# Performance work log

Measured on AMD Instinct MI355X. Metric: run time of the kernel, lower is better.

## Reference

```python
import jax, jax.numpy as jnp
import numpy as np

K1, K2 = 0.01, 0.03
DATA_RANGE = 1.0
EPS = 1e-6


def setup_inputs() -> dict:
    key = jax.random.key(0)
    k1, k2, k3 = jax.random.split(key, 3)
    B, C, H, W = 4, 3, 256, 176
    S, M = 5, 18
    X = jax.random.normal(k1, (B, C, H, W), dtype=jnp.float32)
    Y = jax.random.normal(k2, (B, C, H, W), dtype=jnp.float32)
    bp_mask = jax.random.uniform(k3, (B, S, M, H, W), dtype=jnp.float32)
    return {"X": X, "Y": Y, "bp_mask": bp_mask}


def reference(X, Y, bp_mask):
    # Rescale from [-1, 1] to [0, 1]
    X = (X + 1.0) / 2.0
    Y = (Y + 1.0) / 2.0
    C1 = (K1 * DATA_RANGE) ** 2
    C2 = (K2 * DATA_RANGE) ** 2

    # Normalized mask weights: [B, S, M, H, W]
    msum = bp_mask.sum(axis=(-2, -1), keepdims=True)
    w = bp_mask / (msum + EPS)

    # Masked first / second moments -> [B, S, M, C], no repeated 6D tensors
    mu1 = jnp.einsum('bchw,bsmhw->bsmc', X, w)
    mu2 = jnp.einsum('bchw,bsmhw->bsmc', Y, w)
    mu11 = jnp.einsum('bchw,bsmhw->bsmc', X * X, w)
    mu22 = jnp.einsum('bchw,bsmhw->bsmc', Y * Y, w)
    mu12 = jnp.einsum('bchw,bsmhw->bsmc', X * Y, w)

    mu1_sq = mu1 * mu1
    mu2_sq = mu2 * mu2
    mu1_mu2 = mu1 * mu2
    sigma1_sq = mu11 - mu1_sq
    sigma2_sq = mu22 - mu2_sq
    sigma12 = mu12 - mu1_mu2

    cs = (2.0 * sigma12 + C2) / (sigma1_sq + sigma2_sq + C2)
    ssim = (2.0 * mu1_mu2 + C1) / (mu1_sq + mu2_sq + C1) * cs
    # nonnegative_ssim=True
    ssim = jax.nn.relu(ssim)
    cs = jax.nn.relu(cs)

    # Mean over merged (M, C) axis -> [B, S]
    cs_batch = cs.mean(axis=(2, 3))
    ssim_batch = ssim.mean(axis=(2, 3))

    msssim = jnp.prod(cs_batch[:, :-1], axis=1) * ssim_batch[:, -1]
    return msssim.mean()
```

## Files before the change

### kernel.cpp

```cpp
#include <hip/hip_runtime.h>

#define B_  4
#define C_  3
#define S_  5
#define M_  18
#define HW  45056
#define HW4 (HW/4)
#define SPLIT 4
#define TPB 256
#define CHUNK4 (HW4/SPLIT)
#define ITERS (CHUNK4/TPB)
#define NPLANE (B_*S_*M_)

#define ACC1(WC, XC, YC, c) do { \
    float xs = fmaf((XC), 0.5f, 0.5f); \
    float ys = fmaf((YC), 0.5f, 0.5f); \
    float wx = (WC) * xs; \
    float wy = (WC) * ys; \
    a1[c]  = fmaf((WC), xs, a1[c]); \
    a2[c]  = fmaf((WC), ys, a2[c]); \
    a11[c] = fmaf(wx, xs, a11[c]); \
    a22[c] = fmaf(wy, ys, a22[c]); \
    a12[c] = fmaf(wx, ys, a12[c]); \
  } while (0)

__global__ __launch_bounds__(TPB) void moments_kernel(
    const float4* __restrict__ X, const float4* __restrict__ Y,
    const float4* __restrict__ Mk, float* __restrict__ part) {
  int bid   = blockIdx.x;
  int plane = bid / SPLIT;
  int chunk = bid - plane * SPLIT;
  int b     = plane / (S_ * M_);

  const float4* mp = Mk + (size_t)plane * HW4;
  const float4* xp = X  + (size_t)b * (C_ * HW4);
  const float4* yp = Y  + (size_t)b * (C_ * HW4);

  int base = chunk * CHUNK4 + (int)threadIdx.x;

  float aW = 0.f;
  float a1[C_], a2[C_], a11[C_], a22[C_], a12[C_];
#pragma unroll
  for (int c = 0; c < C_; ++c) { a1[c]=a2[c]=a11[c]=a22[c]=a12[c]=0.f; }

#pragma unroll
  for (int it = 0; it < ITERS; ++it) {
    int i = base + it * TPB;
    float4 w = mp[i];
    aW += (w.x + w.y) + (w.z + w.w);
#pragma unroll
    for (int c = 0; c < C_; ++c) {
      float4 xv = xp[c * HW4 + i];
      float4 yv = yp[c * HW4 + i];
      ACC1(w.x, xv.x, yv.x, c);
      ACC1(w.y, xv.y, yv.y, c);
      ACC1(w.z, xv.z, yv.z, c);
      ACC1(w.w, xv.w, yv.w, c);
    }
  }

  float v[16];
  v[0] = aW;
#pragma unroll
  for (int c = 0; c < C_; ++c) {
    v[1 + c*5 + 0] = a1[c];
    v[1 + c*5 + 1] = a2[c];
    v[1 + c*5 + 2] = a11[c];
    v[1 + c*5 + 3] = a22[c];
    v[1 + c*5 + 4] = a12[c];
  }

#pragma unroll
  for (int off = 32; off > 0; off >>= 1) {
#pragma unroll
    for (int j = 0; j < 16; ++j) v[j] += __shfl_xor(v[j], off);
  }

  __shared__ float red[TPB/64][16];
  int lane = threadIdx.x & 63;
  int wv   = threadIdx.x >> 6;
  if (lane == 0) {
#pragma unroll
    for (int j = 0; j < 16; ++j) red[wv][j] = v[j];
  }
  __syncthreads();
  if (threadIdx.x < 16) {
    float s = (red[0][threadIdx.x] + red[1][threadIdx.x]) +
              (red[2][threadIdx.x] + red[3][threadIdx.x]);
    part[(size_t)bid * 16 + threadIdx.x] = s;
  }
}

__global__ __launch_bounds__(384) void finalize_kernel(
    const float* __restrict__ part, float* __restrict__ out) {
  __shared__ float csS[NPLANE], ssS[NPLANE];
  __shared__ double csb[B_*S_], ssb[B_*S_];
  int t = threadIdx.x;

  if (t < NPLANE) {
    double s[16];
#pragma unroll
    for (int j = 0; j < 16; ++j) s[j] = 0.0;
    for (int ch = 0; ch < SPLIT; ++ch) {
      const float* p = part + (size_t)(t * SPLIT + ch) * 16;
#pragma unroll
      for (int j = 0; j < 16; ++j) s[j] += (double)p[j];
    }
    const double C1d = 1e-4, C2d = 9e-4;
    double inv = 1.0 / (s[0] + 1e-6);
    double csAcc = 0.0, ssAcc = 0.0;
#pragma unroll
    for (int c = 0; c < C_; ++c) {
      double mu1  = s[1 + c*5 + 0] * inv;
      double mu2  = s[1 + c*5 + 1] * inv;
      double mu11 = s[1 + c*5 + 2] * inv;
      double mu22 = s[1 + c*5 + 3] * inv;
      double mu12 = s[1 + c*5 + 4] * inv;
      double m1s = mu1*mu1, m2s = mu2*mu2, m12 = mu1*mu2;
      double sig1  = mu11 - m1s;
      double sig2  = mu22 - m2s;
      double sig12 = mu12 - m12;
      double cs   = (2.0*sig12 + C2d) / (sig1 + sig2 + C2d);
      double ssim = (2.0*m12 + C1d) / (m1s + m2s + C1d) * cs;
      if (cs   < 0.0) cs   = 0.0;
      if (ssim < 0.0) ssim = 0.0;
      csAcc += cs; ssAcc += ssim;
    }
    csS[t] = (float)csAcc;
    ssS[t] = (float)ssAcc;
  }
  __syncthreads();

  if (t < B_*S_) {
    double cb = 0.0, sb = 0.0;
    for (int m = 0; m < M_; ++m) { cb += (double)csS[t*M_ + m]; sb += (double)ssS[t*M_ + m]; }
    csb[t] = cb / (double)(M_*C_);
    ssb[t] = sb / (double)(M_*C_);
  }
  __syncthreads();

  if (t == 0) {
    double acc = 0.0;
    for (int b = 0; b < B_; ++b) {
      double p = ssb[b*S_ + (S_-1)];
      for (int s = 0; s < S_-1; ++s) p *= csb[b*S_ + s];
      acc += p;
    }
    out[0] = (float)(acc / (double)B_);
  }
}

extern "C" void kernel_launch(void* const* d_in, const int* in_sizes, int n_in,
                              void* d_out, int out_size, void* d_ws, size_t ws_size,
                              hipStream_t stream) {
  (void)in_sizes; (void)n_in; (void)out_size; (void)ws_size;
  const float4* X  = (const float4*)d_in[0];
  const float4* Y  = (const float4*)d_in[1];
  const float4* Mk = (const float4*)d_in[2];
  float* part = (float*)d_ws;
  float* out  = (float*)d_out;

  hipLaunchKernelGGL(moments_kernel, dim3(NPLANE*SPLIT), dim3(TPB), 0, stream,
                     X, Y, Mk, part);
  hipLaunchKernelGGL(finalize_kernel, dim3(1), dim3(384), 0, stream, part, out);
}
```

Measured before the change: 117.8 us.

## Process three mask planes per block to reuse X/Y loads

Each block now handles a group of three mask planes, so X and Y loads and their rescaling are shared across three planes instead of being reloaded for each one. The split count rises from 4 to 11, which keeps the grid size similar, and the finalize kernel reindexes the partial sums to match. The cost is higher register pressure from 48 accumulators per thread, longer shuffle reductions, and fewer loop iterations per thread.

```diff
diff --git a/kernel.cpp b/kernel.cpp
--- a/kernel.cpp
+++ b/kernel.cpp
@@ -6,88 +6,94 @@
 #define M_  18
 #define HW  45056
 #define HW4 (HW/4)
-#define SPLIT 4
+#define G_  3
+#define GPBS (M_/G_)
+#define NGROUP (B_*S_*GPBS)
+#define SPLIT 11
 #define TPB 256
 #define CHUNK4 (HW4/SPLIT)
 #define ITERS (CHUNK4/TPB)
+#define NV (G_*16)
 #define NPLANE (B_*S_*M_)
-
-#define ACC1(WC, XC, YC, c) do { \
-    float xs = fmaf((XC), 0.5f, 0.5f); \
-    float ys = fmaf((YC), 0.5f, 0.5f); \
-    float wx = (WC) * xs; \
-    float wy = (WC) * ys; \
-    a1[c]  = fmaf((WC), xs, a1[c]); \
-    a2[c]  = fmaf((WC), ys, a2[c]); \
-    a11[c] = fmaf(wx, xs, a11[c]); \
-    a22[c] = fmaf(wy, ys, a22[c]); \
-    a12[c] = fmaf(wx, ys, a12[c]); \
-  } while (0)
 
 __global__ __launch_bounds__(TPB) void moments_kernel(
     const float4* __restrict__ X, const float4* __restrict__ Y,
     const float4* __restrict__ Mk, float* __restrict__ part) {
   int bid   = blockIdx.x;
-  int plane = bid / SPLIT;
-  int chunk = bid - plane * SPLIT;
-  int b     = plane / (S_ * M_);
+  int g     = bid / SPLIT;
+  int chunk = bid - g * SPLIT;
+  int bs    = g / GPBS;
+  int gm    = g - bs * GPBS;
+  int b     = bs / S_;
 
-  const float4* mp = Mk + (size_t)plane * HW4;
+  const float4* mp = Mk + (size_t)(bs * M_ + gm * G_) * HW4;
   const float4* xp = X  + (size_t)b * (C_ * HW4);
   const float4* yp = Y  + (size_t)b * (C_ * HW4);
 
   int base = chunk * CHUNK4 + (int)threadIdx.x;
 
-  float aW = 0.f;
-  float a1[C_], a2[C_], a11[C_], a22[C_], a12[C_];
+  float acc[NV];
 #pragma unroll
-  for (int c = 0; c < C_; ++c) { a1[c]=a2[c]=a11[c]=a22[c]=a12[c]=0.f; }
+  for (int j = 0; j < NV; ++j) acc[j] = 0.f;
 
 #pragma unroll
   for (int it = 0; it < ITERS; ++it) {
     int i = base + it * TPB;
-    float4 w = mp[i];
-    aW += (w.x + w.y) + (w.z + w.w);
+    float4 wv[G_], xv[C_], yv[C_];
+#pragma unroll
+    for (int j = 0; j < G_; ++j) wv[j] = mp[j * HW4 + i];
+#pragma unroll
+    for (int c = 0; c < C_; ++c) { xv[c] = xp[c * HW4 + i]; yv[c] = yp[c * HW4 + i]; }
+
+    float xs[C_][4], ys[C_][4];
 #pragma unroll
     for (int c = 0; c < C_; ++c) {
-      float4 xv = xp[c * HW4 + i];
-      float4 yv = yp[c * HW4 + i];
-      ACC1(w.x, xv.x, yv.x, c);
-      ACC1(w.y, xv.y, yv.y, c);
-      ACC1(w.z, xv.z, yv.z, c);
-      ACC1(w.w, xv.w, yv.w, c);
+      xs[c][0] = fmaf(xv[c].x, 0.5f, 0.5f); ys[c][0] = fmaf(yv[c].x, 0.5f, 0.5f);
+      xs[c][1] = fmaf(xv[c].y, 0.5f, 0.5f); ys[c][1] = fmaf(yv[c].y, 0.5f, 0.5f);
+      xs[c][2] = fmaf(xv[c].z, 0.5f, 0.5f); ys[c][2] = fmaf(yv[c].z, 0.5f, 0.5f);
+      xs[c][3] = fmaf(xv[c].w, 0.5f, 0.5f); ys[c][3] = fmaf(yv[c].w, 0.5f, 0.5f);
     }
-  }
 
-  float v[16];
-  v[0] = aW;
 #pragma unroll
-  for (int c = 0; c < C_; ++c) {
-    v[1 + c*5 + 0] = a1[c];
-    v[1 + c*5 + 1] = a2[c];
-    v[1 + c*5 + 2] = a11[c];
-    v[1 + c*5 + 3] = a22[c];
-    v[1 + c*5 + 4] = a12[c];
+    for (int j = 0; j < G_; ++j) {
+      float w4[4] = { wv[j].x, wv[j].y, wv[j].z, wv[j].w };
+      float* a = acc + j * 16;
+#pragma unroll
+      for (int k = 0; k < 4; ++k) {
+        float wk = w4[k];
+        a[0] += wk;
+#pragma unroll
+        for (int c = 0; c < C_; ++c) {
+          float xsv = xs[c][k], ysv = ys[c][k];
+          float wx = wk * xsv, wy = wk * ysv;
+          a[1 + c*5 + 0] = fmaf(wk, xsv, a[1 + c*5 + 0]);
+          a[1 + c*5 + 1] = fmaf(wk, ysv, a[1 + c*5 + 1]);
+          a[1 + c*5 + 2] = fmaf(wx, xsv, a[1 + c*5 + 2]);
+          a[1 + c*5 + 3] = fmaf(wy, ysv, a[1 + c*5 + 3]);
+          a[1 + c*5 + 4] = fmaf(wx, ysv, a[1 + c*5 + 4]);
+        }
+      }
+    }
   }
 
 #pragma unroll
   for (int off = 32; off > 0; off >>= 1) {
 #pragma unroll
-    for (int j = 0; j < 16; ++j) v[j] += __shfl_xor(v[j], off);
+    for (int j = 0; j < NV; ++j) acc[j] += __shfl_xor(acc[j], off);
   }
 
-  __shared__ float red[TPB/64][16];
+  __shared__ float red[TPB/64][NV];
   int lane = threadIdx.x & 63;
-  int wv   = threadIdx.x >> 6;
+  int wv_  = threadIdx.x >> 6;
   if (lane == 0) {
 #pragma unroll
-    for (int j = 0; j < 16; ++j) red[wv][j] = v[j];
+    for (int j = 0; j < NV; ++j) red[wv_][j] = acc[j];
   }
   __syncthreads();
-  if (threadIdx.x < 16) {
+  if (threadIdx.x < NV) {
     float s = (red[0][threadIdx.x] + red[1][threadIdx.x]) +
               (red[2][threadIdx.x] + red[3][threadIdx.x]);
-    part[(size_t)bid * 16 + threadIdx.x] = s;
+    part[(size_t)bid * NV + threadIdx.x] = s;
   }
 }
 
@@ -98,14 +104,21 @@
   int t = threadIdx.x;
 
   if (t < NPLANE) {
+    int bs = t / M_;
+    int m  = t - bs * M_;
+    int gm = m / G_;
+    int j  = m - gm * G_;
+    int g  = bs * GPBS + gm;
+
     double s[16];
 #pragma unroll
-    for (int j = 0; j < 16; ++j) s[j] = 0.0;
+    for (int v = 0; v < 16; ++v) s[v] = 0.0;
     for (int ch = 0; ch < SPLIT; ++ch) {
-      const float* p = part + (size_t)(t * SPLIT + ch) * 16;
+      const float* p = part + (size_t)(g * SPLIT + ch) * NV + j * 16;
 #pragma unroll
-      for (int j = 0; j < 16; ++j) s[j] += (double)p[j];
+      for (int v = 0; v < 16; ++v) s[v] += (double)p[v];
     }
+
     const double C1d = 1e-4, C2d = 9e-4;
     double inv = 1.0 / (s[0] + 1e-6);
     double csAcc = 0.0, ssAcc = 0.0;
@@ -160,7 +173,7 @@
   float* part = (float*)d_ws;
   float* out  = (float*)d_out;
 
-  hipLaunchKernelGGL(moments_kernel, dim3(NPLANE*SPLIT), dim3(TPB), 0, stream,
+  hipLaunchKernelGGL(moments_kernel, dim3(NGROUP*SPLIT), dim3(TPB), 0, stream,
                      X, Y, Mk, part);
   hipLaunchKernelGGL(finalize_kernel, dim3(1), dim3(384), 0, stream, part, out);
 }
```

Result: slower. 121.0 us (+2.7%).

## Group six mask planes per block to share X/Y loads, fuse finalize via last-block atomic

Applied to the files above, without the earlier changes.

Each block now holds six waves, and each wave handles a different mask plane over the same spatial chunk. The X/Y reads for that chunk are therefore shared across planes through cache rather than reloaded for every plane. Each wave writes its own partial directly, and a global atomic counter lets the last block run the finalize step, which removes the second kernel launch. The cost is an added memset, an atomic and threadfences per block, and a finalize that runs serially at the tail of the grid.

```diff
diff --git a/kernel.cpp b/kernel.cpp
--- a/kernel.cpp
+++ b/kernel.cpp
@@ -4,70 +4,75 @@
 #define C_  3
 #define S_  5
 #define M_  18
-#define HW  45056
-#define HW4 (HW/4)
-#define SPLIT 4
-#define TPB 256
+#define HW4 11264
+#define G_  6
+#define NGRP (M_/G_)
+#define SPLIT 8
 #define CHUNK4 (HW4/SPLIT)
-#define ITERS (CHUNK4/TPB)
+#define WITER (CHUNK4/64)
+#define TPB (G_*64)
 #define NPLANE (B_*S_*M_)
+#define NBLK (B_*S_*NGRP*SPLIT)
+#define PART_OFF 64
 
-#define ACC1(WC, XC, YC, c) do { \
-    float xs = fmaf((XC), 0.5f, 0.5f); \
-    float ys = fmaf((YC), 0.5f, 0.5f); \
-    float wx = (WC) * xs; \
-    float wy = (WC) * ys; \
-    a1[c]  = fmaf((WC), xs, a1[c]); \
-    a2[c]  = fmaf((WC), ys, a2[c]); \
-    a11[c] = fmaf(wx, xs, a11[c]); \
-    a22[c] = fmaf(wy, ys, a22[c]); \
-    a12[c] = fmaf(wx, ys, a12[c]); \
-  } while (0)
+__global__ __launch_bounds__(TPB) void fused_kernel(
+    const float4* __restrict__ X, const float4* __restrict__ Y,
+    const float4* __restrict__ Mk, float* __restrict__ ws,
+    float* __restrict__ out) {
+  float* part = ws + PART_OFF;
+  unsigned int* cnt = (unsigned int*)ws;
 
-__global__ __launch_bounds__(TPB) void moments_kernel(
-    const float4* __restrict__ X, const float4* __restrict__ Y,
-    const float4* __restrict__ Mk, float* __restrict__ part) {
   int bid   = blockIdx.x;
-  int plane = bid / SPLIT;
-  int chunk = bid - plane * SPLIT;
-  int b     = plane / (S_ * M_);
+  int g     = bid / SPLIT;
+  int chunk = bid - g * SPLIT;
+  int bs    = g / NGRP;
+  int gm    = g - bs * NGRP;
+  int b     = bs / S_;
+  int wv    = threadIdx.x >> 6;
+  int lane  = threadIdx.x & 63;
+  int plane = bs * M_ + gm * G_ + wv;
 
   const float4* mp = Mk + (size_t)plane * HW4;
   const float4* xp = X  + (size_t)b * (C_ * HW4);
   const float4* yp = Y  + (size_t)b * (C_ * HW4);
 
-  int base = chunk * CHUNK4 + (int)threadIdx.x;
+  int base = chunk * CHUNK4 + lane;
 
-  float aW = 0.f;
-  float a1[C_], a2[C_], a11[C_], a22[C_], a12[C_];
+  float v[16];
 #pragma unroll
-  for (int c = 0; c < C_; ++c) { a1[c]=a2[c]=a11[c]=a22[c]=a12[c]=0.f; }
+  for (int j = 0; j < 16; ++j) v[j] = 0.f;
 
 #pragma unroll
-  for (int it = 0; it < ITERS; ++it) {
-    int i = base + it * TPB;
+  for (int it = 0; it < WITER; ++it) {
+    int i = base + it * 64;
     float4 w = mp[i];
-    aW += (w.x + w.y) + (w.z + w.w);
+    float4 xv[C_], yv[C_];
 #pragma unroll
-    for (int c = 0; c < C_; ++c) {
-      float4 xv = xp[c * HW4 + i];
-      float4 yv = yp[c * HW4 + i];
-      ACC1(w.x, xv.x, yv.x, c);
-      ACC1(w.y, xv.y, yv.y, c);
-      ACC1(w.z, xv.z, yv.z, c);
-      ACC1(w.w, xv.w, yv.w, c);
+    for (int c = 0; c < C_; ++c) { xv[c] = xp[c * HW4 + i]; yv[c] = yp[c * HW4 + i]; }
+
+    float w4[4] = { w.x, w.y, w.z, w.w };
+    float x4[C_][4] = { {xv[0].x, xv[0].y, xv[0].z, xv[0].w},
+                        {xv[1].x, xv[1].y, xv[1].z, xv[1].w},
+                        {xv[2].x, xv[2].y, xv[2].z, xv[2].w} };
+    float y4[C_][4] = { {yv[0].x, yv[0].y, yv[0].z, yv[0].w},
+                        {yv[1].x, yv[1].y, yv[1].z, yv[1].w},
+                        {yv[2].x, yv[2].y, yv[2].z, yv[2].w} };
+#pragma unroll
+    for (int k = 0; k < 4; ++k) {
+      float wk = w4[k];
+      v[0] += wk;
+#pragma unroll
+      for (int c = 0; c < C_; ++c) {
+        float xs = fmaf(x4[c][k], 0.5f, 0.5f);
+        float ys = fmaf(y4[c][k], 0.5f, 0.5f);
+        float wx = wk * xs, wy = wk * ys;
+        v[1 + c*5 + 0] = fmaf(wk, xs, v[1 + c*5 + 0]);
+        v[1 + c*5 + 1] = fmaf(wk, ys, v[1 + c*5 + 1]);
+        v[1 + c*5 + 2] = fmaf(wx, xs, v[1 + c*5 + 2]);
+        v[1 + c*5 + 3] = fmaf(wy, ys, v[1 + c*5 + 3]);
+        v[1 + c*5 + 4] = fmaf(wx, ys, v[1 + c*5 + 4]);
+      }
     }
-  }
-
-  float v[16];
-  v[0] = aW;
-#pragma unroll
-  for (int c = 0; c < C_; ++c) {
-    v[1 + c*5 + 0] = a1[c];
-    v[1 + c*5 + 1] = a2[c];
-    v[1 + c*5 + 2] = a11[c];
-    v[1 + c*5 + 3] = a22[c];
-    v[1 + c*5 + 4] = a12[c];
   }
 
 #pragma unroll
@@ -76,23 +81,25 @@
     for (int j = 0; j < 16; ++j) v[j] += __shfl_xor(v[j], off);
   }
 
-  __shared__ float red[TPB/64][16];
-  int lane = threadIdx.x & 63;
-  int wv   = threadIdx.x >> 6;
   if (lane == 0) {
-#pragma unroll
-    for (int j = 0; j < 16; ++j) red[wv][j] = v[j];
+    float4* dst = (float4*)(part + (size_t)(plane * SPLIT + chunk) * 16);
+    dst[0] = make_float4(v[0],  v[1],  v[2],  v[3]);
+    dst[1] = make_float4(v[4],  v[5],  v[6],  v[7]);
+    dst[2] = make_float4(v[8],  v[9],  v[10], v[11]);
+    dst[3] = make_float4(v[12], v[13], v[14], v[15]);
+  }
+
+  __shared__ unsigned int isLast;
+  __syncthreads();
+  if (threadIdx.x == 0) {
+    __threadfence();
+    unsigned int ret = atomicAdd(cnt, 1u);
+    isLast = (ret == (unsigned int)(NBLK - 1)) ? 1u : 0u;
   }
   __syncthreads();
-  if (threadIdx.x < 16) {
-    float s = (red[0][threadIdx.x] + red[1][threadIdx.x]) +
-              (red[2][threadIdx.x] + red[3][threadIdx.x]);
-    part[(size_t)bid * 16 + threadIdx.x] = s;
-  }
-}
+  if (!isLast) return;
+  __threadfence();
 
-__global__ __launch_bounds__(384) void finalize_kernel(
-    const float* __restrict__ part, float* __restrict__ out) {
   __shared__ float csS[NPLANE], ssS[NPLANE];
   __shared__ double csb[B_*S_], ssb[B_*S_];
   int t = threadIdx.x;
@@ -141,9 +148,9 @@
 
   if (t == 0) {
     double acc = 0.0;
-    for (int b = 0; b < B_; ++b) {
-      double p = ssb[b*S_ + (S_-1)];
-      for (int s = 0; s < S_-1; ++s) p *= csb[b*S_ + s];
+    for (int bb = 0; bb < B_; ++bb) {
+      double p = ssb[bb*S_ + (S_-1)];
+      for (int s = 0; s < S_-1; ++s) p *= csb[bb*S_ + s];
       acc += p;
     }
     out[0] = (float)(acc / (double)B_);
@@ -157,10 +164,10 @@
   const float4* X  = (const float4*)d_in[0];
   const float4* Y  = (const float4*)d_in[1];
   const float4* Mk = (const float4*)d_in[2];
-  float* part = (float*)d_ws;
-  float* out  = (float*)d_out;
+  float* ws  = (float*)d_ws;
+  float* out = (float*)d_out;
 
-  hipLaunchKernelGGL(moments_kernel, dim3(NPLANE*SPLIT), dim3(TPB), 0, stream,
-                     X, Y, Mk, part);
-  hipLaunchKernelGGL(finalize_kernel, dim3(1), dim3(384), 0, stream, part, out);
+  hipMemsetAsync(d_ws, 0, 4, stream);
+  hipLaunchKernelGGL(fused_kernel, dim3(NBLK), dim3(TPB), 0, stream,
+                     X, Y, Mk, ws, out);
 }
```

Result: slower. 138.4 us (+17.5%).
